# Kernel optimization log

Hardware: AMD Instinct MI355X
Metric: run time of the kernel (lower is better)

Reference implementation:

```python
import jax, jax.numpy as jnp
import numpy as np
from jax import lax

LEVEL = 128  # level_num

def _bn(x, g, b, m, v):
    # inference-mode BatchNorm, channel axis = 1
    sh = (1, -1) + (1,) * (x.ndim - 2)
    return (x - m.reshape(sh)) * (g.reshape(sh) * lax.rsqrt(v.reshape(sh) + 1e-5)) + b.reshape(sh)

def _leaky(a):
    return jnp.where(a > 0, a, 0.01 * a)

def _l2n(a):
    return a / jnp.maximum(jnp.linalg.norm(a, axis=1, keepdims=True), 1e-12)

def _resize_bilinear_ac(x, oh, ow):
    # bilinear, align_corners=True, NCHW
    n, c, h, w = x.shape
    ys = jnp.linspace(0.0, h - 1.0, oh)
    xs = jnp.linspace(0.0, w - 1.0, ow)
    y0 = jnp.floor(ys).astype(jnp.int32)
    x0 = jnp.floor(xs).astype(jnp.int32)
    y1 = jnp.minimum(y0 + 1, h - 1)
    x1 = jnp.minimum(x0 + 1, w - 1)
    wy = (ys - y0)[:, None]
    wx = (xs - x0)[None, :]
    Y0, Y1, X0, X1 = y0[:, None], y1[:, None], x0[None, :], x1[None, :]
    return (x[:, :, Y0, X0] * (1 - wy) * (1 - wx) + x[:, :, Y0, X1] * (1 - wy) * wx
            + x[:, :, Y1, X0] * wy * (1 - wx) + x[:, :, Y1, X1] * wy * wx)

def _forward(x, conv1_w, bn1_g, bn1_b, bn1_m, bn1_v, conv2_w, f1_w, f2_w, f2_g, f2_b, f2_m, f2_v,
             out1_w, out1_g, out1_b, out1_m, out1_v, k_w, q_w, v_w, out_w, out_g, out_b, out_m, out_v):
    # conv1: 3x3 conv + BN + LeakyReLU
    y = lax.conv_general_dilated(x, conv1_w, (1, 1), 'SAME', dimension_numbers=('NCHW', 'OIHW', 'NCHW'))
    y = _leaky(_bn(y, bn1_g, bn1_b, bn1_m, bn1_v))
    # conv2: 1x1 conv, 256->128
    x2 = jnp.einsum('nchw,oc->nohw', y, conv2_w)
    N, C, H, W = x2.shape  # C = 128
    x_ave = x2.mean(axis=(2, 3), keepdims=True)  # [N,C,1,1]
    cos = (_l2n(x_ave) * _l2n(x2)).sum(1)        # [N,H,W]
    sh, sw = H // 3, W // 3
    L = sh * sw
    # H,W divisible by 3 -> adaptive_avg_pool2d is identity
    cs = cos.reshape(N, 3, sh, 3, sw).transpose(0, 1, 3, 2, 4).reshape(N, 9, L).transpose(0, 2, 1)  # [N,L,9]
    # LBP bit packing vs center (index 4); weight 0 at index 4 (strict > gives 0 there)
    bits = (cs > cs[:, :, 4:5]).astype(x.dtype)
    wts = jnp.array([1, 2, 4, 8, 0, 16, 32, 64, 128], dtype=x.dtype)
    code = (bits * wts).sum(-1)  # [N,L]
    mn = code.min(-1, keepdims=True)
    mx = code.max(-1, keepdims=True)
    code = (code - mn) / (mx - mn)
    cmin = code.min(-1, keepdims=True)
    cmax = code.max(-1, keepdims=True)
    qlv = (2 * jnp.arange(LEVEL, dtype=x.dtype) + 1) / (2 * LEVEL) * (cmax - cmin) + cmin  # [N,LEVEL]
    inter = (qlv[:, 1] - qlv[:, 0])[:, None, None]  # [N,1,1]
    quant = 1 - jnp.abs(qlv[:, None, :] - code[:, :, None])  # [N,L,LEVEL]
    quant = jnp.where(quant > 1 - inter, quant, 0.0)
    sta = quant.sum(1)                                       # [N,LEVEL]
    sta = sta / sta.sum(-1, keepdims=True)
    sta2 = jnp.stack([qlv, sta], axis=1)                     # [N,2,LEVEL]
    h1 = _leaky(jnp.einsum('ncl,oc->nol', sta2, f1_w))       # f1: 2->64
    h2 = jax.nn.relu(_bn(jnp.einsum('ncl,oc->nol', h1, f2_w), f2_g, f2_b, f2_m, f2_v))  # f2: 64->128
    xa = jnp.broadcast_to(x_ave[:, :, 0, 0][:, :, None], (N, C, LEVEL))
    s = jnp.concatenate([h2, xa], axis=1)                    # [N,256,LEVEL]
    s = jax.nn.relu(_bn(jnp.einsum('ncl,oc->nol', s, out1_w), out1_g, out1_b, out1_m, out1_v))
    k = jnp.einsum('ncl,oc->nol', s, k_w)
    q = jnp.einsum('ncl,oc->nol', s, q_w)
    v = jnp.einsum('ncl,oc->nol', s, v_w)
    w = jax.nn.softmax(jnp.einsum('ncl,ncm->nlm', k, q), axis=-1)  # bmm(k^T, q)
    f = jnp.einsum('nlm,ncm->ncl', w, v)                            # bmm(w, v^T) then transpose
    f = jax.nn.relu(_bn(jnp.einsum('ncl,oc->nol', f, out_w), out_g, out_b, out_m, out_v))
    out = jnp.einsum('ncl,npl->ncp', f, quant).reshape(N, 256, sh, sh)  # bmm(f, quant^T)
    return _resize_bilinear_ac(out, H, W)

def setup_inputs() -> dict:
    key = jax.random.key(0)
    ks = jax.random.split(key, 16)
    f32 = jnp.float32
    def nrm(k, shape, s=0.05):
        return s * jax.random.normal(k, shape, f32)
    def bnp(k, c):
        k1, k2, k3, k4 = jax.random.split(k, 4)
        return (1.0 + 0.1 * jax.random.normal(k1, (c,), f32),
                0.1 * jax.random.normal(k2, (c,), f32),
                0.1 * jax.random.normal(k3, (c,), f32),
                jax.random.uniform(k4, (c,), f32, 0.5, 1.5))
    d = {}
    d['x'] = jax.random.normal(ks[0], (32, 512, 48, 48), f32)
    d['conv1_w'] = nrm(ks[1], (256, 512, 3, 3))
    d['bn1_g'], d['bn1_b'], d['bn1_m'], d['bn1_v'] = bnp(ks[2], 256)
    d['conv2_w'] = nrm(ks[3], (128, 256))
    d['f1_w'] = nrm(ks[4], (64, 2), 0.3)
    d['f2_w'] = nrm(ks[5], (128, 64), 0.1)
    d['f2_g'], d['f2_b'], d['f2_m'], d['f2_v'] = bnp(ks[6], 128)
    d['out1_w'] = nrm(ks[7], (256, 256))
    d['out1_g'], d['out1_b'], d['out1_m'], d['out1_v'] = bnp(ks[8], 256)
    d['k_w'] = nrm(ks[9], (256, 256))
    d['q_w'] = nrm(ks[10], (256, 256))
    d['v_w'] = nrm(ks[11], (256, 256))
    d['out_w'] = nrm(ks[12], (256, 256))
    d['out_g'], d['out_b'], d['out_m'], d['out_v'] = bnp(ks[13], 256)
    return d

def reference(x, conv1_w, bn1_g, bn1_b, bn1_m, bn1_v, conv2_w, f1_w, f2_w, f2_g, f2_b, f2_m, f2_v,
              out1_w, out1_g, out1_b, out1_m, out1_v, k_w, q_w, v_w, out_w, out_g, out_b, out_m, out_v):
    return _forward(x, conv1_w, bn1_g, bn1_b, bn1_m, bn1_v, conv2_w, f1_w, f2_w, f2_g, f2_b, f2_m, f2_v,
                    out1_w, out1_g, out1_b, out1_m, out1_v, k_w, q_w, v_w, out_w, out_g, out_b, out_m, out_v)
```

## Files before the change

### kernel.cpp

```cpp
#include <hip/hip_runtime.h>
#include <math.h>

#define N_IMG 32
#define P2304 2304
#define CIN 512
#define CMID 256
#define C2 128
#define LEV 128

typedef _Float16 half8 __attribute__((ext_vector_type(8)));
typedef float f32x16 __attribute__((ext_vector_type(16)));

__device__ __forceinline__ float wredSum(float v){
#pragma unroll
  for (int o = 32; o > 0; o >>= 1) v += __shfl_down(v, o, 64);
  return v;
}
__device__ __forceinline__ float wredMax(float v){
#pragma unroll
  for (int o = 32; o > 0; o >>= 1) v = fmaxf(v, __shfl_down(v, o, 64));
  return v;
}
__device__ __forceinline__ float wredMin(float v){
#pragma unroll
  for (int o = 32; o > 0; o >>= 1) v = fminf(v, __shfl_down(v, o, 64));
  return v;
}

__global__ void prep_w1_kernel(const float* __restrict__ w1,
                               uint4* __restrict__ Wh, uint4* __restrict__ Wl){
  int fid = blockIdx.x * 256 + threadIdx.x;
  int lam = fid & 63;
  int c32 = (fid >> 6) & 3;
  int cot = (fid >> 8) & 1;
  int kt  = fid >> 9;
  int co = cot * 128 + c32 * 32 + (lam & 31);
  half8 vh, vl;
#pragma unroll
  for (int j = 0; j < 8; ++j){
    int k = kt * 16 + ((lam >> 5) << 3) + j;
    int r = k >> 9;
    int ci = k & 511;
    float v = w1[co * (CIN * 9) + ci * 9 + r];
    _Float16 h = (_Float16)v;
    vh[j] = h;
    vl[j] = (_Float16)((v - (float)h) * 2048.0f);
  }
  Wh[fid] = *(uint4*)&vh;
  Wl[fid] = *(uint4*)&vl;
}

__global__ void prep_w2_kernel(const float* __restrict__ w2,
                               uint4* __restrict__ Wh, uint4* __restrict__ Wl){
  int fid = blockIdx.x * 256 + threadIdx.x;
  int lam = fid & 63;
  int c32 = (fid >> 6) & 3;
  int kt  = fid >> 8;
  int co = c32 * 32 + (lam & 31);
  half8 vh, vl;
#pragma unroll
  for (int j = 0; j < 8; ++j){
    int k = kt * 16 + ((lam >> 5) << 3) + j;
    float v = w2[co * CMID + k];
    _Float16 h = (_Float16)v;
    vh[j] = h;
    vl[j] = (_Float16)((v - (float)h) * 2048.0f);
  }
  Wh[fid] = *(uint4*)&vh;
  Wl[fid] = *(uint4*)&vl;
}

__global__ void prep_bn_kernel(const float* __restrict__ g1, const float* __restrict__ b1,
                               const float* __restrict__ m1, const float* __restrict__ v1,
                               float* __restrict__ s1, float* __restrict__ t1){
  int c = threadIdx.x;
  float s = g1[c] * (1.0f / sqrtf(v1[c] + 1e-5f));
  s1[c] = s;
  t1[c] = b1[c] - m1[c] * s;
}

template<int R, int CPT, int COTN, bool BN>
__global__ __launch_bounds__(256, 2) void conv_mfma_kernel(
    const float* __restrict__ in, const uint4* __restrict__ Wh, const uint4* __restrict__ Wl,
    const float* __restrict__ s1, const float* __restrict__ t1, float* __restrict__ out)
{
  __shared__ _Float16 Ah[2048], Al[2048], Bh[2048], Bl[2048];
  const int t = threadIdx.x;
  const int lam = t & 63;
  const int g = t >> 6;

  int n, pt_blk, cot;
  if (COTN == 2){
    int xcd = blockIdx.x & 7;
    int rest = blockIdx.x >> 3;
    n = xcd * 4 + rest / 36;
    int inner = rest % 36;
    pt_blk = inner % 18;
    cot = inner / 18;
  } else {
    pt_blk = blockIdx.x % 18;
    cot = 0;
    n = blockIdx.x / 18;
  }
  const int pbase = pt_blk * 128;
  const int cobase = cot * 128;

  const int khi = lam >> 5;
  const int pp = (g << 5) + (lam & 31);
  const int p = pbase + pp;
  const int ph = p / 48, pw = p - ph * 48;
  const float* in_n = in + (size_t)n * CPT * P2304;

  const int KTPR = CPT / 16;
  const int KT = R * KTPR;

  f32x16 acc_hh[2][2], acc_x[2][2];
#pragma unroll
  for (int a = 0; a < 2; ++a)
#pragma unroll
    for (int b = 0; b < 2; ++b){
#pragma unroll
      for (int e = 0; e < 16; ++e){ acc_hh[a][b][e] = 0.f; acc_x[a][b][e] = 0.f; }
    }

  uint4 rAh, rAl;
  float rB[8];

#define LOAD_AB(KTV)                                                          \
  {                                                                           \
    int kt_ = (KTV);                                                          \
    int fi = ((kt_ * COTN + cot) * 4 + g) * 64 + lam;                         \
    rAh = Wh[fi];                                                             \
    rAl = Wl[fi];                                                             \
    int r_ = kt_ / KTPR;                                                      \
    int it_ = kt_ - r_ * KTPR;                                                \
    int dh_ = (R == 1) ? 0 : (r_ / 3 - 1);                                    \
    int dw_ = (R == 1) ? 0 : (r_ - (r_ / 3) * 3 - 1);                         \
    int hh_ = ph + dh_, ww_ = pw + dw_;                                       \
    bool valid_ = ((unsigned)hh_ < 48u) & ((unsigned)ww_ < 48u);              \
    const float* src_ = in_n + (valid_ ? (hh_ * 48 + ww_) : 0)                \
                        + (size_t)((khi << 3) + (it_ << 4)) * P2304;          \
    _Pragma("unroll")                                                         \
    for (int j = 0; j < 8; ++j) rB[j] = valid_ ? src_[j * P2304] : 0.0f;      \
  }

  LOAD_AB(0);

  for (int kt = 0; kt < KT; ++kt){
    half8 vh, vl;
#pragma unroll
    for (int j = 0; j < 8; ++j){
      float v = rB[j];
      _Float16 h = (_Float16)v;
      vh[j] = h;
      vl[j] = (_Float16)((v - (float)h) * 2048.0f);
    }
    uint4 sAh = rAh, sAl = rAl;
    __syncthreads();
    *(uint4*)&Ah[t * 8] = sAh;
    *(uint4*)&Al[t * 8] = sAl;
    *(half8*)&Bh[t * 8] = vh;
    *(half8*)&Bl[t * 8] = vl;
    __syncthreads();
    if (kt + 1 < KT) LOAD_AB(kt + 1);

    const int ct0 = (g & 1) * 2, pt0 = (g >> 1) * 2;
    half8 fAh[2], fAl[2], fBh[2], fBl[2];
#pragma unroll
    for (int a = 0; a < 2; ++a){
      fAh[a] = *(half8*)&Ah[((ct0 + a) * 64 + lam) * 8];
      fAl[a] = *(half8*)&Al[((ct0 + a) * 64 + lam) * 8];
      fBh[a] = *(half8*)&Bh[((pt0 + a) * 64 + lam) * 8];
      fBl[a] = *(half8*)&Bl[((pt0 + a) * 64 + lam) * 8];
    }
#pragma unroll
    for (int a = 0; a < 2; ++a)
#pragma unroll
      for (int b = 0; b < 2; ++b){
        acc_hh[a][b] = __builtin_amdgcn_mfma_f32_32x32x16_f16(fAh[a], fBh[b], acc_hh[a][b], 0, 0, 0);
        acc_x[a][b]  = __builtin_amdgcn_mfma_f32_32x32x16_f16(fAh[a], fBl[b], acc_x[a][b], 0, 0, 0);
        acc_x[a][b]  = __builtin_amdgcn_mfma_f32_32x32x16_f16(fAl[a], fBh[b], acc_x[a][b], 0, 0, 0);
      }
  }
#undef LOAD_AB

  const int M = COTN * 128;
#pragma unroll
  for (int a = 0; a < 2; ++a){
    const int ctile = (g & 1) * 2 + a;
#pragma unroll
    for (int b = 0; b < 2; ++b){
      const int ptile = (g >> 1) * 2 + b;
      const int pg = pbase + ptile * 32 + (lam & 31);
#pragma unroll
      for (int rg = 0; rg < 16; ++rg){
        const int row = (rg & 3) + 8 * (rg >> 2) + 4 * (lam >> 5);
        const int co = cobase + ctile * 32 + row;
        float val = acc_hh[a][b][rg] + acc_x[a][b][rg] * (1.0f / 2048.0f);
        if (BN){
          val = val * s1[co] + t1[co];
          val = val > 0.f ? val : 0.01f * val;
        }
        out[((size_t)n * M + co) * P2304 + pg] = val;
      }
    }
  }
}

__global__ void xave_kernel(const float* __restrict__ x2, float* __restrict__ xave){
  __shared__ float red[4];
  int nc = blockIdx.x, t = threadIdx.x;
  const float* row = x2 + nc * P2304;
  float s = 0.f;
#pragma unroll
  for (int i = 0; i < 9; i++) s += row[t + 256 * i];
  float w = wredSum(s);
  if ((t & 63) == 0) red[t >> 6] = w;
  __syncthreads();
  if (t == 0) xave[nc] = (red[0] + red[1] + red[2] + red[3]) * (1.0f / 2304.0f);
}

__global__ void xan_kernel(const float* __restrict__ xave, float* __restrict__ xan){
  __shared__ float red[2];
  int n = blockIdx.x, t = threadIdx.x;
  float v = xave[n * 128 + t];
  float w = wredSum(v * v);
  if ((t & 63) == 0) red[t >> 6] = w;
  __syncthreads();
  float norm = fmaxf(sqrtf(red[0] + red[1]), 1e-12f);
  xan[n * 128 + t] = v / norm;
}

__global__ void cos_kernel(const float* __restrict__ x2, const float* __restrict__ xan,
                           float* __restrict__ cosb){
  int idx = blockIdx.x * 256 + threadIdx.x;
  if (idx >= N_IMG * P2304) return;
  int n = idx / P2304;
  int p = idx - n * P2304;
  const float* xp = x2 + n * C2 * P2304 + p;
  const float* an = xan + n * 128;
  float dot = 0.f, ss = 0.f;
  for (int c = 0; c < 128; c++){
    float v = xp[c * P2304];
    dot += an[c] * v;
    ss  += v * v;
  }
  cosb[idx] = dot / fmaxf(sqrtf(ss), 1e-12f);
}

__global__ void lbp_kernel(const float* __restrict__ cosb, float* __restrict__ code,
                           float* __restrict__ qlv){
  __shared__ float red[4];
  int n = blockIdx.x;
  int l = threadIdx.x;
  int ir = l >> 4, ic = l & 15;
  const float* cn = cosb + n * P2304;
  float cs4 = cn[(16 + ir) * 48 + (16 + ic)];
  const float wts[9] = {1.f, 2.f, 4.f, 8.f, 0.f, 16.f, 32.f, 64.f, 128.f};
  float codev = 0.f;
#pragma unroll
  for (int j = 0; j < 9; j++){
    int jr = j / 3, jc = j - 3 * (j / 3);
    float vv = cn[(jr * 16 + ir) * 48 + (jc * 16 + ic)];
    if (vv > cs4) codev += wts[j];
  }
  float w;
  w = wredMin(codev);
  if ((l & 63) == 0) red[l >> 6] = w;
  __syncthreads();
  float mn = fminf(fminf(red[0], red[1]), fminf(red[2], red[3]));
  __syncthreads();
  w = wredMax(codev);
  if ((l & 63) == 0) red[l >> 6] = w;
  __syncthreads();
  float mx = fmaxf(fmaxf(red[0], red[1]), fmaxf(red[2], red[3]));
  __syncthreads();
  float cd = (codev - mn) / (mx - mn);
  w = wredMin(cd);
  if ((l & 63) == 0) red[l >> 6] = w;
  __syncthreads();
  float cmin = fminf(fminf(red[0], red[1]), fminf(red[2], red[3]));
  __syncthreads();
  w = wredMax(cd);
  if ((l & 63) == 0) red[l >> 6] = w;
  __syncthreads();
  float cmax = fmaxf(fmaxf(red[0], red[1]), fmaxf(red[2], red[3]));
  code[n * 256 + l] = cd;
  if (l < 128){
    float tmp = (float)(2 * l + 1) * (1.0f / 256.0f);
    qlv[n * 128 + l] = tmp * (cmax - cmin) + cmin;
  }
}

__global__ void quant_kernel(const float* __restrict__ code, const float* __restrict__ qlv,
                             float* __restrict__ quantT){
  __shared__ float cs[256];
  __shared__ float qs[128];
  int n = blockIdx.x, t = threadIdx.x;
  cs[t] = code[n * 256 + t];
  if (t < 128) qs[t] = qlv[n * 128 + t];
  __syncthreads();
  float thr = 1.0f - (qs[1] - qs[0]);
  float* dst = quantT + n * LEV * 256;
#pragma unroll 4
  for (int i = 0; i < 128; i++){
    int v = t + 256 * i;
    int lv = v >> 8;
    int p = v & 255;
    float qq = 1.0f - fabsf(qs[lv] - cs[p]);
    dst[v] = (qq > thr) ? qq : 0.f;
  }
}

__global__ void sta_kernel(const float* __restrict__ quantT, float* __restrict__ sta){
  __shared__ float red[2];
  int n = blockIdx.x, i = threadIdx.x;
  const float* qr = quantT + (n * LEV + i) * 256;
  float s = 0.f;
  for (int p = 0; p < 256; p++) s += qr[p];
  float w = wredSum(s);
  if ((i & 63) == 0) red[i >> 6] = w;
  __syncthreads();
  float tot = red[0] + red[1];
  sta[n * 128 + i] = s / tot;
}

__global__ void h1_kernel(const float* __restrict__ f1w, const float* __restrict__ qlv,
                          const float* __restrict__ sta, float* __restrict__ h1){
  int idx = blockIdx.x * 256 + threadIdx.x;
  if (idx >= N_IMG * 64 * 128) return;
  int l = idx & 127;
  int n = idx >> 13;
  int o = (idx >> 7) & 63;
  float a = f1w[o * 2] * qlv[n * 128 + l] + f1w[o * 2 + 1] * sta[n * 128 + l];
  h1[idx] = a > 0.f ? a : 0.01f * a;
}

__global__ void gemm_w_kernel(const float* __restrict__ Wm, const float* __restrict__ B,
                              float* __restrict__ Cout, int Cdim, int O, int total, int mode,
                              const float* __restrict__ g, const float* __restrict__ bb,
                              const float* __restrict__ mm, const float* __restrict__ vv){
  int idx = blockIdx.x * 256 + threadIdx.x;
  if (idx >= total) return;
  int per_n = (O >> 2) << 7;
  int n = idx / per_n;
  int rem = idx - n * per_n;
  int o0 = (rem >> 7) << 2;
  int l = rem & 127;
  const float* Bn = B + (n * Cdim) * 128 + l;
  const float* w0 = Wm + (o0 + 0) * Cdim;
  const float* w1 = Wm + (o0 + 1) * Cdim;
  const float* w2 = Wm + (o0 + 2) * Cdim;
  const float* w3 = Wm + (o0 + 3) * Cdim;
  float a0 = 0, a1 = 0, a2 = 0, a3 = 0;
  for (int c = 0; c < Cdim; c++){
    float bv = Bn[c * 128];
    a0 += w0[c] * bv; a1 += w1[c] * bv; a2 += w2[c] * bv; a3 += w3[c] * bv;
  }
  float av[4] = {a0, a1, a2, a3};
#pragma unroll
  for (int j = 0; j < 4; j++){
    int o = o0 + j;
    float val = av[j];
    if (mode == 1){
      float s = g[o] * (1.0f / sqrtf(vv[o] + 1e-5f));
      val = (val - mm[o]) * s + bb[o];
      val = fmaxf(val, 0.f);
    }
    Cout[(n * O + o) * 128 + l] = val;
  }
}

__global__ void concat_kernel(const float* __restrict__ h2, const float* __restrict__ xave,
                              float* __restrict__ s){
  int idx = blockIdx.x * 256 + threadIdx.x;
  if (idx >= N_IMG * 256 * 128) return;
  int l = idx & 127;
  int c = (idx >> 7) & 255;
  int n = idx >> 15;
  s[idx] = (c < 128) ? h2[(n * 128 + c) * 128 + l] : xave[n * 128 + (c - 128)];
}

__global__ void attn_sc_kernel(const float* __restrict__ k, const float* __restrict__ q,
                               float* __restrict__ sc){
  int idx = blockIdx.x * 256 + threadIdx.x;
  if (idx >= N_IMG * 32 * 128) return;
  int m = idx & 127;
  int l0 = ((idx >> 7) & 31) << 2;
  int n = idx >> 12;
  const float* kn = k + n * 256 * 128;
  const float* qn = q + n * 256 * 128 + m;
  float a0 = 0, a1 = 0, a2 = 0, a3 = 0;
  for (int c = 0; c < 256; c++){
    float qv = qn[c * 128];
    const float* kr = kn + c * 128 + l0;
    a0 += kr[0] * qv; a1 += kr[1] * qv; a2 += kr[2] * qv; a3 += kr[3] * qv;
  }
  float* dst = sc + (n * 128 + l0) * 128 + m;
  dst[0] = a0; dst[128] = a1; dst[256] = a2; dst[384] = a3;
}

__global__ void softmax_kernel(float* __restrict__ sc){
  __shared__ float red[2];
  int row = blockIdx.x;
  int t = threadIdx.x;
  float v = sc[row * 128 + t];
  float w = wredMax(v);
  if ((t & 63) == 0) red[t >> 6] = w;
  __syncthreads();
  float mx = fmaxf(red[0], red[1]);
  float e = expf(v - mx);
  float s = wredSum(e);
  __syncthreads();
  if ((t & 63) == 0) red[t >> 6] = s;
  __syncthreads();
  sc[row * 128 + t] = e / (red[0] + red[1]);
}

__global__ void transpose_sc_kernel(const float* __restrict__ sc, float* __restrict__ scT){
  int idx = blockIdx.x * 256 + threadIdx.x;
  if (idx >= N_IMG * 128 * 128) return;
  int l = idx & 127;
  int m = (idx >> 7) & 127;
  int n = idx >> 14;
  scT[idx] = sc[(n * 128 + l) * 128 + m];
}

__global__ void attn_f_kernel(const float* __restrict__ vb, const float* __restrict__ scT,
                              float* __restrict__ f){
  int idx = blockIdx.x * 256 + threadIdx.x;
  if (idx >= N_IMG * 64 * 128) return;
  int l = idx & 127;
  int c0 = ((idx >> 7) & 63) << 2;
  int n = idx >> 13;
  const float* vn = vb + (n * 256 + c0) * 128;
  const float* sn = scT + n * 128 * 128 + l;
  float a0 = 0, a1 = 0, a2 = 0, a3 = 0;
  for (int m = 0; m < 128; m++){
    float sv = sn[m * 128];
    a0 += vn[m] * sv; a1 += vn[128 + m] * sv; a2 += vn[256 + m] * sv; a3 += vn[384 + m] * sv;
  }
  float* dst = f + (n * 256 + c0) * 128 + l;
  dst[0] = a0; dst[128] = a1; dst[256] = a2; dst[384] = a3;
}

__global__ void final_kernel(const float* __restrict__ g, const float* __restrict__ quantT,
                             float* __restrict__ outs){
  int idx = blockIdx.x * 256 + threadIdx.x;
  if (idx >= N_IMG * 64 * 256) return;
  int p = idx & 255;
  int c0 = ((idx >> 8) & 63) << 2;
  int n = idx >> 14;
  const float* gn = g + (n * 256 + c0) * 128;
  const float* qn = quantT + (n * LEV) * 256 + p;
  float a0 = 0, a1 = 0, a2 = 0, a3 = 0;
  for (int lv = 0; lv < 128; lv++){
    float qv = qn[lv * 256];
    a0 += gn[lv] * qv; a1 += gn[128 + lv] * qv; a2 += gn[256 + lv] * qv; a3 += gn[384 + lv] * qv;
  }
  float* dst = outs + (n * 256 + c0) * 256 + p;
  dst[0] = a0; dst[256] = a1; dst[512] = a2; dst[768] = a3;
}

__global__ void resize_kernel(const float* __restrict__ outs, float* __restrict__ dout){
  int idx = blockIdx.x * 256 + threadIdx.x;
  if (idx >= N_IMG * 256 * P2304) return;
  int ow = idx % 48;
  int tmp = idx / 48;
  int oh = tmp % 48;
  int nc = tmp / 48;
  const float* src = outs + nc * 256;
  float fy = oh * (15.0f / 47.0f);
  float fx = ow * (15.0f / 47.0f);
  int y0 = (int)fy;
  int x0 = (int)fx;
  int y1 = min(y0 + 1, 15);
  int x1 = min(x0 + 1, 15);
  float wy = fy - (float)y0;
  float wx = fx - (float)x0;
  float v00 = src[y0 * 16 + x0], v01 = src[y0 * 16 + x1];
  float v10 = src[y1 * 16 + x0], v11 = src[y1 * 16 + x1];
  dout[idx] = v00 * (1.f - wy) * (1.f - wx) + v01 * (1.f - wy) * wx
            + v10 * wy * (1.f - wx) + v11 * wy * wx;
}

extern "C" void kernel_launch(void* const* d_in, const int* in_sizes, int n_in,
                              void* d_out, int out_size, void* d_ws, size_t ws_size,
                              hipStream_t stream)
{
  const float* x       = (const float*)d_in[0];
  const float* conv1_w = (const float*)d_in[1];
  const float* bn1_g   = (const float*)d_in[2];
  const float* bn1_b   = (const float*)d_in[3];
  const float* bn1_m   = (const float*)d_in[4];
  const float* bn1_v   = (const float*)d_in[5];
  const float* conv2_w = (const float*)d_in[6];
  const float* f1_w    = (const float*)d_in[7];
  const float* f2_w    = (const float*)d_in[8];
  const float* f2_g    = (const float*)d_in[9];
  const float* f2_b    = (const float*)d_in[10];
  const float* f2_m    = (const float*)d_in[11];
  const float* f2_v    = (const float*)d_in[12];
  const float* out1_w  = (const float*)d_in[13];
  const float* out1_g  = (const float*)d_in[14];
  const float* out1_b  = (const float*)d_in[15];
  const float* out1_m  = (const float*)d_in[16];
  const float* out1_v  = (const float*)d_in[17];
  const float* k_w     = (const float*)d_in[18];
  const float* q_w     = (const float*)d_in[19];
  const float* v_w     = (const float*)d_in[20];
  const float* out_w   = (const float*)d_in[21];
  const float* out_g   = (const float*)d_in[22];
  const float* out_b   = (const float*)d_in[23];
  const float* out_m   = (const float*)d_in[24];
  const float* out_v   = (const float*)d_in[25];

  float* ws = (float*)d_ws;
  float* dout = (float*)d_out;

  float* w_y   = ws;
  float* w_x2  = ws + 18874368;
  float* w_W1h = ws + 28311552;
  float* w_W1l = ws + 28901376;
  float* w_W2h = ws + 29491200;
  float* w_W2l = ws + 29507584;
  float* w_s1  = ws + 29523968;
  float* w_t1  = ws + 29524224;
  float* w_xave = w_y + 0;
  float* w_xan  = w_y + 4096;
  float* w_cos  = w_y + 8192;
  float* w_code = w_y + 81920;
  float* w_qlv  = w_y + 90112;
  float* w_sta  = w_y + 94208;
  float* w_quant= w_y + 98304;
  float* w_h1   = w_y + 1146880;
  float* w_h2   = w_y + 1409024;
  float* w_s    = w_y + 1933312;
  float* w_k    = w_y + 2981888;
  float* w_q    = w_y + 4030464;
  float* w_v    = w_y + 5079040;
  float* w_sc   = w_y + 6127616;
  float* w_scT  = w_y + 6651904;
  float* w_f    = w_y + 7176192;
  float* w_g    = w_y + 8224768;
  float* w_outs = w_y + 9273344;
  float* w_s2   = w_y + 11370496;

  prep_w1_kernel<<<576, 256, 0, stream>>>(conv1_w, (uint4*)w_W1h, (uint4*)w_W1l);
  prep_w2_kernel<<<16, 256, 0, stream>>>(conv2_w, (uint4*)w_W2h, (uint4*)w_W2l);
  prep_bn_kernel<<<1, 256, 0, stream>>>(bn1_g, bn1_b, bn1_m, bn1_v, w_s1, w_t1);

  conv_mfma_kernel<9, 512, 2, true><<<1152, 256, 0, stream>>>(
      x, (const uint4*)w_W1h, (const uint4*)w_W1l, w_s1, w_t1, w_y);
  conv_mfma_kernel<1, 256, 1, false><<<576, 256, 0, stream>>>(
      w_y, (const uint4*)w_W2h, (const uint4*)w_W2l, w_s1, w_t1, w_x2);

  xave_kernel<<<4096, 256, 0, stream>>>(w_x2, w_xave);
  xan_kernel<<<32, 128, 0, stream>>>(w_xave, w_xan);
  cos_kernel<<<288, 256, 0, stream>>>(w_x2, w_xan, w_cos);
  lbp_kernel<<<32, 256, 0, stream>>>(w_cos, w_code, w_qlv);
  quant_kernel<<<32, 256, 0, stream>>>(w_code, w_qlv, w_quant);
  sta_kernel<<<32, 128, 0, stream>>>(w_quant, w_sta);
  h1_kernel<<<1024, 256, 0, stream>>>(f1_w, w_qlv, w_sta, w_h1);
  gemm_w_kernel<<<512, 256, 0, stream>>>(f2_w, w_h1, w_h2, 64, 128, N_IMG * 32 * 128, 1,
                                         f2_g, f2_b, f2_m, f2_v);
  concat_kernel<<<4096, 256, 0, stream>>>(w_h2, w_xave, w_s);
  gemm_w_kernel<<<1024, 256, 0, stream>>>(out1_w, w_s, w_s2, 256, 256, N_IMG * 64 * 128, 1,
                                          out1_g, out1_b, out1_m, out1_v);
  gemm_w_kernel<<<1024, 256, 0, stream>>>(k_w, w_s2, w_k, 256, 256, N_IMG * 64 * 128, 0,
                                          nullptr, nullptr, nullptr, nullptr);
  gemm_w_kernel<<<1024, 256, 0, stream>>>(q_w, w_s2, w_q, 256, 256, N_IMG * 64 * 128, 0,
                                          nullptr, nullptr, nullptr, nullptr);
  gemm_w_kernel<<<1024, 256, 0, stream>>>(v_w, w_s2, w_v, 256, 256, N_IMG * 64 * 128, 0,
                                          nullptr, nullptr, nullptr, nullptr);
  attn_sc_kernel<<<512, 256, 0, stream>>>(w_k, w_q, w_sc);
  softmax_kernel<<<4096, 128, 0, stream>>>(w_sc);
  transpose_sc_kernel<<<2048, 256, 0, stream>>>(w_sc, w_scT);
  attn_f_kernel<<<1024, 256, 0, stream>>>(w_v, w_scT, w_f);
  gemm_w_kernel<<<1024, 256, 0, stream>>>(out_w, w_f, w_g, 256, 256, N_IMG * 64 * 128, 1,
                                          out_g, out_b, out_m, out_v);
  final_kernel<<<2048, 256, 0, stream>>>(w_g, w_quant, w_outs);
  resize_kernel<<<73728, 256, 0, stream>>>(w_outs, dout);
}
```

Before: 1.584 ms.

## Double-buffer LDS tiles and process two K-steps per barrier in conv MFMA

Restructures the conv MFMA main loop to use double-buffered shared memory holding two 16-wide K slices per stage. Global loads for the next stage are issued before compute, and the fp16 split and LDS store are interleaved between the two MFMA groups. This cuts barriers from two per K-step to one per two K-steps. It doubles LDS use (64KB per block) and register pressure, which may cut occupancy below the two blocks per SM requested by launch bounds. Out-of-bounds loads are now clamped and masked instead of predicated.

```diff
diff --git a/kernel.cpp b/kernel.cpp
--- a/kernel.cpp
+++ b/kernel.cpp
@@ -84,7 +84,8 @@
     const float* __restrict__ in, const uint4* __restrict__ Wh, const uint4* __restrict__ Wl,
     const float* __restrict__ s1, const float* __restrict__ t1, float* __restrict__ out)
 {
-  __shared__ _Float16 Ah[2048], Al[2048], Bh[2048], Bl[2048];
+  __shared__ _Float16 Abuf[2][2][2][2048];
+  __shared__ _Float16 Bbuf[2][2][2][2048];
   const int t = threadIdx.x;
   const int lam = t & 63;
   const int g = t >> 6;
@@ -111,8 +112,8 @@
   const int ph = p / 48, pw = p - ph * 48;
   const float* in_n = in + (size_t)n * CPT * P2304;
 
-  const int KTPR = CPT / 16;
-  const int KT = R * KTPR;
+  const int S = (R * CPT) / 32;
+  const int KTPT = CPT / 16;
 
   f32x16 acc_hh[2][2], acc_x[2][2];
 #pragma unroll
@@ -123,66 +124,94 @@
       for (int e = 0; e < 16; ++e){ acc_hh[a][b][e] = 0.f; acc_x[a][b][e] = 0.f; }
     }
 
-  uint4 rAh, rAl;
-  float rB[8];
-
-#define LOAD_AB(KTV)                                                          \
+  uint4 rAh[2], rAl[2];
+  float rB[16];
+  bool vmask;
+
+#define ISSUE(SV)                                                             \
   {                                                                           \
-    int kt_ = (KTV);                                                          \
-    int fi = ((kt_ * COTN + cot) * 4 + g) * 64 + lam;                         \
-    rAh = Wh[fi];                                                             \
-    rAl = Wl[fi];                                                             \
-    int r_ = kt_ / KTPR;                                                      \
-    int it_ = kt_ - r_ * KTPR;                                                \
+    int s_ = (SV);                                                            \
+    _Pragma("unroll")                                                         \
+    for (int kf = 0; kf < 2; ++kf){                                           \
+      int fi = (((2 * s_ + kf) * COTN + cot) * 4 + g) * 64 + lam;             \
+      rAh[kf] = Wh[fi];                                                       \
+      rAl[kf] = Wl[fi];                                                       \
+    }                                                                         \
+    int r_ = (R == 1) ? 0 : ((2 * s_) / KTPT);                                \
+    int cbase_ = ((2 * s_) % KTPT) * 16;                                      \
     int dh_ = (R == 1) ? 0 : (r_ / 3 - 1);                                    \
     int dw_ = (R == 1) ? 0 : (r_ - (r_ / 3) * 3 - 1);                         \
     int hh_ = ph + dh_, ww_ = pw + dw_;                                       \
-    bool valid_ = ((unsigned)hh_ < 48u) & ((unsigned)ww_ < 48u);              \
-    const float* src_ = in_n + (valid_ ? (hh_ * 48 + ww_) : 0)                \
-                        + (size_t)((khi << 3) + (it_ << 4)) * P2304;          \
+    vmask = ((unsigned)hh_ < 48u) & ((unsigned)ww_ < 48u);                    \
+    int hc_ = min(max(hh_, 0), 47), wc_ = min(max(ww_, 0), 47);               \
+    const float* src_ = in_n + hc_ * 48 + wc_                                 \
+                        + (size_t)(cbase_ + khi * 8) * P2304;                 \
     _Pragma("unroll")                                                         \
-    for (int j = 0; j < 8; ++j) rB[j] = valid_ ? src_[j * P2304] : 0.0f;      \
-  }
-
-  LOAD_AB(0);
-
-  for (int kt = 0; kt < KT; ++kt){
-    half8 vh, vl;
-#pragma unroll
-    for (int j = 0; j < 8; ++j){
-      float v = rB[j];
-      _Float16 h = (_Float16)v;
-      vh[j] = h;
-      vl[j] = (_Float16)((v - (float)h) * 2048.0f);
-    }
-    uint4 sAh = rAh, sAl = rAl;
+    for (int kf = 0; kf < 2; ++kf)                                            \
+      _Pragma("unroll")                                                       \
+      for (int j = 0; j < 8; ++j)                                             \
+        rB[kf * 8 + j] = src_[(kf * 16 + j) * P2304];                         \
+  }
+
+#define STASH(NXT)                                                            \
+  {                                                                           \
+    _Pragma("unroll")                                                         \
+    for (int kf = 0; kf < 2; ++kf){                                           \
+      *(uint4*)&Abuf[NXT][kf][0][t * 8] = rAh[kf];                            \
+      *(uint4*)&Abuf[NXT][kf][1][t * 8] = rAl[kf];                            \
+      half8 vh, vl;                                                           \
+      _Pragma("unroll")                                                       \
+      for (int j = 0; j < 8; ++j){                                            \
+        float v = vmask ? rB[kf * 8 + j] : 0.0f;                              \
+        _Float16 h = (_Float16)v;                                             \
+        vh[j] = h;                                                            \
+        vl[j] = (_Float16)((v - (float)h) * 2048.0f);                         \
+      }                                                                       \
+      *(half8*)&Bbuf[NXT][kf][0][t * 8] = vh;                                 \
+      *(half8*)&Bbuf[NXT][kf][1][t * 8] = vl;                                 \
+    }                                                                         \
+  }
+
+#define COMPUTE(CUR, KF)                                                      \
+  {                                                                           \
+    const int ct0 = (g & 1) * 2, pt0 = (g >> 1) * 2;                          \
+    half8 fAh[2], fAl[2], fBh[2], fBl[2];                                     \
+    _Pragma("unroll")                                                         \
+    for (int a = 0; a < 2; ++a){                                              \
+      fAh[a] = *(half8*)&Abuf[CUR][KF][0][(ct0 + a) * 512 + lam * 8];         \
+      fAl[a] = *(half8*)&Abuf[CUR][KF][1][(ct0 + a) * 512 + lam * 8];         \
+      fBh[a] = *(half8*)&Bbuf[CUR][KF][0][(pt0 + a) * 512 + lam * 8];         \
+      fBl[a] = *(half8*)&Bbuf[CUR][KF][1][(pt0 + a) * 512 + lam * 8];         \
+    }                                                                         \
+    _Pragma("unroll")                                                         \
+    for (int a = 0; a < 2; ++a)                                               \
+      _Pragma("unroll")                                                       \
+      for (int b = 0; b < 2; ++b){                                            \
+        acc_hh[a][b] = __builtin_amdgcn_mfma_f32_32x32x16_f16(                \
+            fAh[a], fBh[b], acc_hh[a][b], 0, 0, 0);                           \
+        acc_x[a][b] = __builtin_amdgcn_mfma_f32_32x32x16_f16(                 \
+            fAh[a], fBl[b], acc_x[a][b], 0, 0, 0);                            \
+        acc_x[a][b] = __builtin_amdgcn_mfma_f32_32x32x16_f16(                 \
+            fAl[a], fBh[b], acc_x[a][b], 0, 0, 0);                            \
+      }                                                                       \
+  }
+
+  ISSUE(0);
+  STASH(0);
+  __syncthreads();
+
+  for (int s = 0; s < S; ++s){
+    const int cur = s & 1, nxt = cur ^ 1;
+    const bool more = (s + 1 < S);
+    if (more) ISSUE(s + 1);
+    COMPUTE(cur, 0);
+    if (more) STASH(nxt);
+    COMPUTE(cur, 1);
     __syncthreads();
-    *(uint4*)&Ah[t * 8] = sAh;
-    *(uint4*)&Al[t * 8] = sAl;
-    *(half8*)&Bh[t * 8] = vh;
-    *(half8*)&Bl[t * 8] = vl;
-    __syncthreads();
-    if (kt + 1 < KT) LOAD_AB(kt + 1);
-
-    const int ct0 = (g & 1) * 2, pt0 = (g >> 1) * 2;
-    half8 fAh[2], fAl[2], fBh[2], fBl[2];
-#pragma unroll
-    for (int a = 0; a < 2; ++a){
-      fAh[a] = *(half8*)&Ah[((ct0 + a) * 64 + lam) * 8];
-      fAl[a] = *(half8*)&Al[((ct0 + a) * 64 + lam) * 8];
-      fBh[a] = *(half8*)&Bh[((pt0 + a) * 64 + lam) * 8];
-      fBl[a] = *(half8*)&Bl[((pt0 + a) * 64 + lam) * 8];
-    }
-#pragma unroll
-    for (int a = 0; a < 2; ++a)
-#pragma unroll
-      for (int b = 0; b < 2; ++b){
-        acc_hh[a][b] = __builtin_amdgcn_mfma_f32_32x32x16_f16(fAh[a], fBh[b], acc_hh[a][b], 0, 0, 0);
-        acc_x[a][b]  = __builtin_amdgcn_mfma_f32_32x32x16_f16(fAh[a], fBl[b], acc_x[a][b], 0, 0, 0);
-        acc_x[a][b]  = __builtin_amdgcn_mfma_f32_32x32x16_f16(fAl[a], fBh[b], acc_x[a][b], 0, 0, 0);
-      }
-  }
-#undef LOAD_AB
+  }
+#undef ISSUE
+#undef STASH
+#undef COMPUTE
 
   const int M = COTN * 128;
 #pragma unroll
```

Result: faster. 1.511 ms (-4.6%).
